# Kernel tuning notes

Measured on AMD Instinct MI355X. Metric: run time of the kernel, lower is better.

## Reference

```python
import jax, jax.numpy as jnp
import numpy as np

N_NODES = 100000


def gcn_conv(x, src, dst, norm, W, b, n_nodes):
    # x: [N, Din]; src/dst: [E'] (with self-loops); norm: [E']
    h = x @ W  # [N, Dout] dense transform first (PyG GCNConv order)
    msgs = h[src] * norm[:, None]  # gather + degree scaling, [E', Dout]
    out = jax.ops.segment_sum(msgs, dst, num_segments=n_nodes)  # scatter-add
    return out + b


def setup_inputs() -> dict:
    key = jax.random.key(0)
    k_x, k_e, k_w1, k_w2 = jax.random.split(key, 4)
    input_dim, hidden_dim = 256, 128
    n_edges = 1600000
    x = jax.random.normal(k_x, (N_NODES, input_dim), dtype=jnp.float32)
    edge_index = jax.random.randint(k_e, (2, n_edges), 0, N_NODES, dtype=jnp.int64)
    # Glorot-style init for conv weights, zeros bias (PyG defaults)
    s1 = (6.0 / (input_dim + hidden_dim)) ** 0.5
    s2 = (6.0 / (hidden_dim + hidden_dim)) ** 0.5
    W1 = jax.random.uniform(k_w1, (input_dim, hidden_dim), jnp.float32, -s1, s1)
    W2 = jax.random.uniform(k_w2, (hidden_dim, hidden_dim), jnp.float32, -s2, s2)
    b1 = jnp.zeros((hidden_dim,), jnp.float32)
    b2 = jnp.zeros((hidden_dim,), jnp.float32)
    return {"x": x, "edge_index": edge_index, "W1": W1, "b1": b1, "W2": W2, "b2": b2}


def reference(x, edge_index, W1, b1, W2, b2):
    n = x.shape[0]
    loops = jnp.arange(n, dtype=edge_index.dtype)
    src = jnp.concatenate([edge_index[0], loops])  # add self-loops
    dst = jnp.concatenate([edge_index[1], loops])
    # symmetric normalization deg^-1/2 (in-degree including self-loops)
    deg = jax.ops.segment_sum(jnp.ones_like(dst, dtype=x.dtype), dst, num_segments=n)
    dinv = jax.lax.rsqrt(deg)
    norm = dinv[src] * dinv[dst]
    # layer 1: GCNConv -> ReLU (dropout is identity in eval mode)
    h = jax.nn.relu(gcn_conv(x, src, dst, norm, W1, b1, n))
    # layer 2
    h = jax.nn.relu(gcn_conv(h, src, dst, norm, W2, b2, n))
    return h
```

## Files before the change

kernel.cpp:

```cpp
#include <hip/hip_runtime.h>
#include <hip/hip_bf16.h>


#define DIN 256
#define DH 128
#define BKT_SHIFT 9
#define BKT_SZ 512

typedef __attribute__((ext_vector_type(8))) short short8;
typedef __attribute__((ext_vector_type(4))) float f32x4;

__device__ __forceinline__ unsigned short f2bf(float f) {
    union { float f; unsigned int i; } c;
    c.f = f;
    unsigned int r = c.i + 0x7FFFu + ((c.i >> 16) & 1u);
    return (unsigned short)(r >> 16);
}
__device__ __forceinline__ float bf_lo(unsigned int u) {
    union { unsigned int i; float f; } c;
    c.i = u << 16;
    return c.f;
}
__device__ __forceinline__ float bf_hi(unsigned int u) {
    union { unsigned int i; float f; } c;
    c.i = u & 0xFFFF0000u;
    return c.f;
}

__global__ void count_k(const int* __restrict__ dst, int* __restrict__ cnt, int e) {
    int i = blockIdx.x * 256 + threadIdx.x;
    if (i < e) atomicAdd(&cnt[dst[i]], 1);
}

__global__ void dinv_k(const int* __restrict__ cnt, float* __restrict__ dinv, int n) {
    int i = blockIdx.x * 256 + threadIdx.x;
    if (i < n) dinv[i] = 1.0f / sqrtf((float)(cnt[i] + 1));
}

__global__ void block_sum_k(const int* __restrict__ cnt, int* __restrict__ bsum, int n) {
    __shared__ int s[256];
    int t = threadIdx.x;
    int i = blockIdx.x * 256 + t;
    s[t] = (i < n) ? cnt[i] : 0;
    __syncthreads();
    for (int off = 128; off > 0; off >>= 1) {
        if (t < off) s[t] += s[t + off];
        __syncthreads();
    }
    if (t == 0) bsum[blockIdx.x] = s[0];
}

__global__ void scan_bsum_k(int* __restrict__ bsum, int nb) {
    __shared__ int s[512];
    int t = threadIdx.x;
    s[t] = (t < nb) ? bsum[t] : 0;
    __syncthreads();
    for (int off = 1; off < 512; off <<= 1) {
        int x = (t >= off) ? s[t - off] : 0;
        __syncthreads();
        s[t] += x;
        __syncthreads();
    }
    if (t < nb) bsum[t] = (t == 0) ? 0 : s[t - 1];
}

__global__ void scan_write_k(const int* __restrict__ cnt, const int* __restrict__ bsum,
                             int* __restrict__ rowptr, int n) {
    __shared__ int s[256];
    int t = threadIdx.x;
    int i = blockIdx.x * 256 + t;
    int c = (i < n) ? cnt[i] : 0;
    s[t] = c;
    __syncthreads();
    for (int off = 1; off < 256; off <<= 1) {
        int x = (t >= off) ? s[t - off] : 0;
        __syncthreads();
        s[t] += x;
        __syncthreads();
    }
    int excl = s[t] - c + bsum[blockIdx.x];
    if (i < n) {
        rowptr[i] = excl;
        if (i == n - 1) rowptr[n] = excl + c;
    }
}

__global__ void init_bcur_k(const int* __restrict__ rowptr, int* __restrict__ bcur, int nbkt) {
    int b = threadIdx.x;
    if (b < nbkt) bcur[b] = rowptr[b << BKT_SHIFT];
}

__global__ void wt_k(const float* __restrict__ W, unsigned short* __restrict__ Wt, int K) {
    int i = blockIdx.x * 256 + threadIdx.x;
    if (i < K * 128) {
        int k = i >> 7, n = i & 127;
        Wt[(size_t)n * K + k] = f2bf(W[i]);
    }
}

__global__ __launch_bounds__(256) void bucket_k(const int* __restrict__ src,
                                                const int* __restrict__ dst,
                                                const float* __restrict__ dinv,
                                                int* __restrict__ bcur,
                                                int2* __restrict__ tmp, int e, int n) {
    __shared__ int hist[256];
    __shared__ int rstart[256];
    int nbkt = (n + BKT_SZ - 1) >> BKT_SHIFT;
    int t = threadIdx.x;
    int nb = gridDim.x;
    int chunk = (e + nb - 1) / nb;
    int beg = blockIdx.x * chunk, end = min(e, beg + chunk);

    hist[t] = 0;
    __syncthreads();
    for (int i = beg + t; i < end; i += 256) atomicAdd(&hist[dst[i] >> BKT_SHIFT], 1);
    __syncthreads();
    int h = hist[t];
    if (t < nbkt && h > 0) rstart[t] = atomicAdd(&bcur[t], h);
    __syncthreads();
    hist[t] = 0;
    __syncthreads();
    for (int i = beg + t; i < end; i += 256) {
        int d = dst[i];
        int b = d >> BKT_SHIFT;
        int o = atomicAdd(&hist[b], 1);
        int s = src[i];
        float w = dinv[s] * dinv[d];
        tmp[rstart[b] + o] = make_int2(s | ((d & (BKT_SZ - 1)) << 20), __float_as_int(w));
    }
}

__global__ __launch_bounds__(1024) void scatter2_k(const int2* __restrict__ tmp,
                                                   const int* __restrict__ rowptr,
                                                   int2* __restrict__ einfo, int n) {
    __shared__ int cur[BKT_SZ];
    int b = blockIdx.x;
    int t = threadIdx.x;
    int lo = b << BKT_SHIFT;
    int hi = min(n, lo + BKT_SZ);
    int nn = hi - lo;
    if (t < nn) cur[t] = rowptr[lo + t];
    __syncthreads();
    int beg = rowptr[lo], end = rowptr[hi];
    for (int i = beg + t; i < end; i += 1024) {
        int2 r = tmp[i];
        int dlow = (r.x >> 20) & (BKT_SZ - 1);
        int pos = atomicAdd(&cur[dlow], 1);
        einfo[pos] = make_int2(r.x & 0xFFFFF, r.y);
    }
}

template <bool A_BF16>
__global__ __launch_bounds__(256) void gemm_mfma(const void* __restrict__ Av,
                                                 const unsigned short* __restrict__ Wt,
                                                 unsigned short* __restrict__ Hb,
                                                 int M, int K) {
    __shared__ unsigned short Bt[16384];
    const int t = threadIdx.x;
    const int w = t >> 6;
    const int lane = t & 63;
    const int l15 = lane & 15;
    const int quad = lane >> 4;
    const int row0 = blockIdx.x * 128 + w * 32;

    const float* Af = (const float*)Av;
    const unsigned short* Ab = (const unsigned short*)Av;

    f32x4 acc[2][8];
#pragma unroll
    for (int rt = 0; rt < 2; ++rt)
#pragma unroll
        for (int ct = 0; ct < 8; ++ct)
#pragma unroll
            for (int j = 0; j < 4; ++j) acc[rt][ct][j] = 0.0f;

    for (int kc = 0; kc < K; kc += 128) {
        if (kc) __syncthreads();
#pragma unroll
        for (int i = 0; i < 8; ++i) {
            int fg = w * 8 + i;
            int ks = fg >> 3, ct = fg & 7;
            int nn = ct * 16 + l15;
            int gk = ks * 32 + quad * 8;
            *(short8*)&Bt[fg * 512 + lane * 8] =
                *(const short8*)(Wt + (size_t)nn * K + kc + gk);
        }
        __syncthreads();
#pragma unroll
        for (int ks = 0; ks < 4; ++ks) {
            int kk = ks * 32 + quad * 8;
            short8 af[2];
#pragma unroll
            for (int rt = 0; rt < 2; ++rt) {
                int row = row0 + rt * 16 + l15;
                if (row < M) {
                    if (A_BF16) {
                        af[rt] = *(const short8*)(Ab + (size_t)row * K + kc + kk);
                    } else {
                        const float* p = Af + (size_t)row * K + kc + kk;
                        float4 x0 = *(const float4*)p;
                        float4 x1 = *(const float4*)(p + 4);
                        af[rt][0] = (short)f2bf(x0.x);
                        af[rt][1] = (short)f2bf(x0.y);
                        af[rt][2] = (short)f2bf(x0.z);
                        af[rt][3] = (short)f2bf(x0.w);
                        af[rt][4] = (short)f2bf(x1.x);
                        af[rt][5] = (short)f2bf(x1.y);
                        af[rt][6] = (short)f2bf(x1.z);
                        af[rt][7] = (short)f2bf(x1.w);
                    }
                } else {
#pragma unroll
                    for (int j = 0; j < 8; ++j) af[rt][j] = 0;
                }
            }
#pragma unroll
            for (int ct = 0; ct < 8; ++ct) {
                short8 bfr = *(const short8*)&Bt[(ks * 8 + ct) * 512 + lane * 8];
                acc[0][ct] = __builtin_amdgcn_mfma_f32_16x16x32_bf16(af[0], bfr, acc[0][ct], 0, 0, 0);
                acc[1][ct] = __builtin_amdgcn_mfma_f32_16x16x32_bf16(af[1], bfr, acc[1][ct], 0, 0, 0);
            }
        }
    }
#pragma unroll
    for (int rt = 0; rt < 2; ++rt)
#pragma unroll
        for (int r = 0; r < 4; ++r) {
            int row = row0 + rt * 16 + quad * 4 + r;
            if (row < M) {
                unsigned short* o = Hb + (size_t)row * 128 + l15;
#pragma unroll
                for (int ct = 0; ct < 8; ++ct) o[ct * 16] = f2bf(acc[rt][ct][r]);
            }
        }
}

template <bool OUT_BF16>
__global__ __launch_bounds__(256) void agg_k(const unsigned short* __restrict__ Hb,
                                             const int* __restrict__ rowptr,
                                             const int2* __restrict__ einfo,
                                             const float* __restrict__ dinv,
                                             const float* __restrict__ bias,
                                             void* __restrict__ out, int n) {
    int v = blockIdx.x * 4 + (threadIdx.x >> 6);
    int lane = threadIdx.x & 63;
    if (v >= n) return;
    int l = lane & 31, half = lane >> 5;
    const uint2* __restrict__ H = (const uint2*)Hb;
    float a0 = 0.f, a1 = 0.f, a2 = 0.f, a3 = 0.f;
    if (half == 0) {
        float dv = dinv[v];
        float self = dv * dv;
        uint2 hv = H[(size_t)v * 32 + l];
        a0 = self * bf_lo(hv.x); a1 = self * bf_hi(hv.x);
        a2 = self * bf_lo(hv.y); a3 = self * bf_hi(hv.y);
    }
    int end = rowptr[v + 1];
    int i = rowptr[v] + half;
    for (; i + 6 < end; i += 8) {
        int2 e0 = einfo[i], e1 = einfo[i + 2], e2 = einfo[i + 4], e3 = einfo[i + 6];
        uint2 v0 = H[(size_t)e0.x * 32 + l];
        uint2 v1 = H[(size_t)e1.x * 32 + l];
        uint2 v2 = H[(size_t)e2.x * 32 + l];
        uint2 v3 = H[(size_t)e3.x * 32 + l];
        float w0 = __int_as_float(e0.y), w1 = __int_as_float(e1.y);
        float w2 = __int_as_float(e2.y), w3 = __int_as_float(e3.y);
        a0 = fmaf(w0, bf_lo(v0.x), a0); a1 = fmaf(w0, bf_hi(v0.x), a1);
        a2 = fmaf(w0, bf_lo(v0.y), a2); a3 = fmaf(w0, bf_hi(v0.y), a3);
        a0 = fmaf(w1, bf_lo(v1.x), a0); a1 = fmaf(w1, bf_hi(v1.x), a1);
        a2 = fmaf(w1, bf_lo(v1.y), a2); a3 = fmaf(w1, bf_hi(v1.y), a3);
        a0 = fmaf(w2, bf_lo(v2.x), a0); a1 = fmaf(w2, bf_hi(v2.x), a1);
        a2 = fmaf(w2, bf_lo(v2.y), a2); a3 = fmaf(w2, bf_hi(v2.y), a3);
        a0 = fmaf(w3, bf_lo(v3.x), a0); a1 = fmaf(w3, bf_hi(v3.x), a1);
        a2 = fmaf(w3, bf_lo(v3.y), a2); a3 = fmaf(w3, bf_hi(v3.y), a3);
    }
    for (; i < end; i += 2) {
        int2 e = einfo[i];
        uint2 vv = H[(size_t)e.x * 32 + l];
        float w = __int_as_float(e.y);
        a0 = fmaf(w, bf_lo(vv.x), a0); a1 = fmaf(w, bf_hi(vv.x), a1);
        a2 = fmaf(w, bf_lo(vv.y), a2); a3 = fmaf(w, bf_hi(vv.y), a3);
    }
    a0 += __shfl_xor(a0, 32);
    a1 += __shfl_xor(a1, 32);
    a2 += __shfl_xor(a2, 32);
    a3 += __shfl_xor(a3, 32);
    if (half == 0) {
        float4 bb = ((const float4*)bias)[l];
        float o0 = fmaxf(a0 + bb.x, 0.f);
        float o1 = fmaxf(a1 + bb.y, 0.f);
        float o2 = fmaxf(a2 + bb.z, 0.f);
        float o3 = fmaxf(a3 + bb.w, 0.f);
        if (OUT_BF16) {
            unsigned int p0 = (unsigned int)f2bf(o0) | ((unsigned int)f2bf(o1) << 16);
            unsigned int p1 = (unsigned int)f2bf(o2) | ((unsigned int)f2bf(o3) << 16);
            ((uint2*)out)[(size_t)v * 32 + l] = make_uint2(p0, p1);
        } else {
            ((float4*)out)[(size_t)v * 32 + l] = make_float4(o0, o1, o2, o3);
        }
    }
}

static inline size_t align_up(size_t x, size_t a) { return (x + a - 1) & ~(a - 1); }

extern "C" void kernel_launch(void* const* d_in, const int* in_sizes, int n_in,
                              void* d_out, int out_size, void* d_ws, size_t ws_size,
                              hipStream_t stream) {
    const float* x  = (const float*)d_in[0];
    const int*   ei = (const int*)d_in[1];
    const float* W1 = (const float*)d_in[2];
    const float* b1 = (const float*)d_in[3];
    const float* W2 = (const float*)d_in[4];
    const float* b2 = (const float*)d_in[5];

    const int N = in_sizes[0] / DIN;
    const int E = in_sizes[1] / 2;
    const int* src = ei;
    const int* dst = ei + E;
    const int NBKT = (N + BKT_SZ - 1) >> BKT_SHIFT;

    char* base = (char*)d_ws;
    size_t off = 0;
    int* cnt = (int*)(base + off);          off = align_up(off + (size_t)N * 4, 256);
    int* rowptr = (int*)(base + off);       off = align_up(off + (size_t)(N + 1) * 4, 256);
    float* dinv = (float*)(base + off);     off = align_up(off + (size_t)N * 4, 256);
    int* bsum = (int*)(base + off);         off = align_up(off + 512 * 4, 256);
    int* bcur = (int*)(base + off);         off = align_up(off + 256 * 4, 256);
    int2* tmp = (int2*)(base + off);        off = align_up(off + (size_t)E * 8, 256);
    int2* einfo = (int2*)(base + off);      off = align_up(off + (size_t)E * 8, 256);
    unsigned short* Wt1 = (unsigned short*)(base + off); off = align_up(off + (size_t)128 * 256 * 2, 256);
    unsigned short* Wt2 = (unsigned short*)(base + off); off = align_up(off + (size_t)128 * 128 * 2, 256);
    unsigned short* hb  = (unsigned short*)(base + off); off = align_up(off + (size_t)N * 128 * 2, 256);
    unsigned short* a1b = (unsigned short*)(base + off); off = align_up(off + (size_t)N * 128 * 2, 256);

    float* out = (float*)d_out;
    const int NB = (N + 255) / 256;

    hipMemsetAsync(cnt, 0, (size_t)N * sizeof(int), stream);
    count_k<<<(E + 255) / 256, 256, 0, stream>>>(dst, cnt, E);
    dinv_k<<<NB, 256, 0, stream>>>(cnt, dinv, N);
    block_sum_k<<<NB, 256, 0, stream>>>(cnt, bsum, N);
    scan_bsum_k<<<1, 512, 0, stream>>>(bsum, NB);
    scan_write_k<<<NB, 256, 0, stream>>>(cnt, bsum, rowptr, N);
    init_bcur_k<<<1, 256, 0, stream>>>(rowptr, bcur, NBKT);
    wt_k<<<(256 * 128 + 255) / 256, 256, 0, stream>>>(W1, Wt1, 256);
    wt_k<<<(128 * 128 + 255) / 256, 256, 0, stream>>>(W2, Wt2, 128);

    bucket_k<<<512, 256, 0, stream>>>(src, dst, dinv, bcur, tmp, E, N);
    scatter2_k<<<NBKT, 1024, 0, stream>>>(tmp, rowptr, einfo, N);

    const int GB = (N + 127) / 128;
    gemm_mfma<false><<<GB, 256, 0, stream>>>(x, Wt1, hb, N, DIN);
    agg_k<true><<<(N + 3) / 4, 256, 0, stream>>>(hb, rowptr, einfo, dinv, b1, a1b, N);
    gemm_mfma<true><<<GB, 256, 0, stream>>>(a1b, Wt2, hb, N, DH);
    agg_k<false><<<(N + 3) / 4, 256, 0, stream>>>(hb, rowptr, einfo, dinv, b2, out, N);
}
```

Measured before the change: 498.3 us.

## Privatize degree counters, fuse small prep kernels, deepen aggregation unroll

Degree counting now spreads atomics across 8 privatized copies of the counter array, indexed by block, to reduce atomic contention. A fused kernel then sums the copies and computes dinv and the block sums in one pass. The two weight-transpose launches are merged into a single kernel. The aggregation loop gains a 16-edge unrolled stage to keep more gathers in flight, at the cost of an 8x larger memset and extra registers.

```diff
diff --git a/kernel.cpp b/kernel.cpp
--- a/kernel.cpp
+++ b/kernel.cpp
@@ -27,21 +27,27 @@
     return c.f;
 }
 
-__global__ void count_k(const int* __restrict__ dst, int* __restrict__ cnt, int e) {
+__global__ void count_k(const int* __restrict__ dst, int* __restrict__ cnt8,
+                        int e, int n) {
     int i = blockIdx.x * 256 + threadIdx.x;
-    if (i < e) atomicAdd(&cnt[dst[i]], 1);
-}
-
-__global__ void dinv_k(const int* __restrict__ cnt, float* __restrict__ dinv, int n) {
-    int i = blockIdx.x * 256 + threadIdx.x;
-    if (i < n) dinv[i] = 1.0f / sqrtf((float)(cnt[i] + 1));
-}
-
-__global__ void block_sum_k(const int* __restrict__ cnt, int* __restrict__ bsum, int n) {
+    if (i < e) atomicAdd(&cnt8[(blockIdx.x & 7) * n + dst[i]], 1);
+}
+
+__global__ __launch_bounds__(256) void dinv_bsum_k(const int* __restrict__ cnt8,
+                                                   int* __restrict__ cnt,
+                                                   float* __restrict__ dinv,
+                                                   int* __restrict__ bsum, int n) {
     __shared__ int s[256];
     int t = threadIdx.x;
     int i = blockIdx.x * 256 + t;
-    s[t] = (i < n) ? cnt[i] : 0;
+    int c = 0;
+    if (i < n) {
+#pragma unroll
+        for (int k = 0; k < 8; ++k) c += cnt8[k * n + i];
+        cnt[i] = c;
+        dinv[i] = 1.0f / sqrtf((float)(c + 1));
+    }
+    s[t] = c;
     __syncthreads();
     for (int off = 128; off > 0; off >>= 1) {
         if (t < off) s[t] += s[t + off];
@@ -90,11 +96,16 @@
     if (b < nbkt) bcur[b] = rowptr[b << BKT_SHIFT];
 }
 
-__global__ void wt_k(const float* __restrict__ W, unsigned short* __restrict__ Wt, int K) {
+__global__ void wt_all_k(const float* __restrict__ W1, const float* __restrict__ W2,
+                         unsigned short* __restrict__ Wt1, unsigned short* __restrict__ Wt2) {
     int i = blockIdx.x * 256 + threadIdx.x;
-    if (i < K * 128) {
+    if (i < 256 * 128) {
         int k = i >> 7, n = i & 127;
-        Wt[(size_t)n * K + k] = f2bf(W[i]);
+        Wt1[(size_t)n * 256 + k] = f2bf(W1[i]);
+    } else if (i < 256 * 128 + 128 * 128) {
+        int j = i - 256 * 128;
+        int k = j >> 7, n = j & 127;
+        Wt2[(size_t)n * 128 + k] = f2bf(W2[j]);
     }
 }
 
@@ -257,6 +268,38 @@
     }
     int end = rowptr[v + 1];
     int i = rowptr[v] + half;
+    for (; i + 14 < end; i += 16) {
+        int2 e0 = einfo[i],      e1 = einfo[i + 2],  e2 = einfo[i + 4],  e3 = einfo[i + 6];
+        int2 e4 = einfo[i + 8],  e5 = einfo[i + 10], e6 = einfo[i + 12], e7 = einfo[i + 14];
+        uint2 v0 = H[(size_t)e0.x * 32 + l];
+        uint2 v1 = H[(size_t)e1.x * 32 + l];
+        uint2 v2 = H[(size_t)e2.x * 32 + l];
+        uint2 v3 = H[(size_t)e3.x * 32 + l];
+        uint2 v4 = H[(size_t)e4.x * 32 + l];
+        uint2 v5 = H[(size_t)e5.x * 32 + l];
+        uint2 v6 = H[(size_t)e6.x * 32 + l];
+        uint2 v7 = H[(size_t)e7.x * 32 + l];
+        float w0 = __int_as_float(e0.y), w1 = __int_as_float(e1.y);
+        float w2 = __int_as_float(e2.y), w3 = __int_as_float(e3.y);
+        float w4 = __int_as_float(e4.y), w5 = __int_as_float(e5.y);
+        float w6 = __int_as_float(e6.y), w7 = __int_as_float(e7.y);
+        a0 = fmaf(w0, bf_lo(v0.x), a0); a1 = fmaf(w0, bf_hi(v0.x), a1);
+        a2 = fmaf(w0, bf_lo(v0.y), a2); a3 = fmaf(w0, bf_hi(v0.y), a3);
+        a0 = fmaf(w1, bf_lo(v1.x), a0); a1 = fmaf(w1, bf_hi(v1.x), a1);
+        a2 = fmaf(w1, bf_lo(v1.y), a2); a3 = fmaf(w1, bf_hi(v1.y), a3);
+        a0 = fmaf(w2, bf_lo(v2.x), a0); a1 = fmaf(w2, bf_hi(v2.x), a1);
+        a2 = fmaf(w2, bf_lo(v2.y), a2); a3 = fmaf(w2, bf_hi(v2.y), a3);
+        a0 = fmaf(w3, bf_lo(v3.x), a0); a1 = fmaf(w3, bf_hi(v3.x), a1);
+        a2 = fmaf(w3, bf_lo(v3.y), a2); a3 = fmaf(w3, bf_hi(v3.y), a3);
+        a0 = fmaf(w4, bf_lo(v4.x), a0); a1 = fmaf(w4, bf_hi(v4.x), a1);
+        a2 = fmaf(w4, bf_lo(v4.y), a2); a3 = fmaf(w4, bf_hi(v4.y), a3);
+        a0 = fmaf(w5, bf_lo(v5.x), a0); a1 = fmaf(w5, bf_hi(v5.x), a1);
+        a2 = fmaf(w5, bf_lo(v5.y), a2); a3 = fmaf(w5, bf_hi(v5.y), a3);
+        a0 = fmaf(w6, bf_lo(v6.x), a0); a1 = fmaf(w6, bf_hi(v6.x), a1);
+        a2 = fmaf(w6, bf_lo(v6.y), a2); a3 = fmaf(w6, bf_hi(v6.y), a3);
+        a0 = fmaf(w7, bf_lo(v7.x), a0); a1 = fmaf(w7, bf_hi(v7.x), a1);
+        a2 = fmaf(w7, bf_lo(v7.y), a2); a3 = fmaf(w7, bf_hi(v7.y), a3);
+    }
     for (; i + 6 < end; i += 8) {
         int2 e0 = einfo[i], e1 = einfo[i + 2], e2 = einfo[i + 4], e3 = einfo[i + 6];
         uint2 v0 = H[(size_t)e0.x * 32 + l];
@@ -321,6 +364,7 @@
 
     char* base = (char*)d_ws;
     size_t off = 0;
+    int* cnt8 = (int*)(base + off);         off = align_up(off + (size_t)8 * N * 4, 256);
     int* cnt = (int*)(base + off);          off = align_up(off + (size_t)N * 4, 256);
     int* rowptr = (int*)(base + off);       off = align_up(off + (size_t)(N + 1) * 4, 256);
     float* dinv = (float*)(base + off);     off = align_up(off + (size_t)N * 4, 256);
@@ -336,15 +380,13 @@
     float* out = (float*)d_out;
     const int NB = (N + 255) / 256;
 
-    hipMemsetAsync(cnt, 0, (size_t)N * sizeof(int), stream);
-    count_k<<<(E + 255) / 256, 256, 0, stream>>>(dst, cnt, E);
-    dinv_k<<<NB, 256, 0, stream>>>(cnt, dinv, N);
-    block_sum_k<<<NB, 256, 0, stream>>>(cnt, bsum, N);
+    hipMemsetAsync(cnt8, 0, (size_t)8 * N * sizeof(int), stream);
+    count_k<<<(E + 255) / 256, 256, 0, stream>>>(dst, cnt8, E, N);
+    dinv_bsum_k<<<NB, 256, 0, stream>>>(cnt8, cnt, dinv, bsum, N);
     scan_bsum_k<<<1, 512, 0, stream>>>(bsum, NB);
     scan_write_k<<<NB, 256, 0, stream>>>(cnt, bsum, rowptr, N);
     init_bcur_k<<<1, 256, 0, stream>>>(rowptr, bcur, NBKT);
-    wt_k<<<(256 * 128 + 255) / 256, 256, 0, stream>>>(W1, Wt1, 256);
-    wt_k<<<(128 * 128 + 255) / 256, 256, 0, stream>>>(W2, Wt2, 128);
+    wt_all_k<<<(256 * 128 + 128 * 128 + 255) / 256, 256, 0, stream>>>(W1, W2, Wt1, Wt2);
 
     bucket_k<<<512, 256, 0, stream>>>(src, dst, dinv, bcur, tmp, E, N);
     scatter2_k<<<NBKT, 1024, 0, stream>>>(tmp, rowptr, einfo, N);
```

Result: slower. 510.3 us (+2.4%).
